# Kernel tuning notes

Measured on AMD Instinct MI355X. Metric: run time of the kernel, lower is better.

Reference implementation:

```python
import jax, jax.numpy as jnp
import numpy as np

NUM_HEADS = 32
NUM_KV_HEADS = 8
HEAD_DIM = 128
ROPE_THETA = 10000.0
NEG_INF = -1e9


def _rope_cos_sin(position_ids, head_dim, dtype):
    # inv_freq: [head_dim/2]
    inv_freq = 1.0 / (ROPE_THETA ** (jnp.arange(0, head_dim, 2, dtype=jnp.float32) / head_dim))
    # freqs: [B, S, head_dim/2]
    freqs = position_ids.astype(jnp.float32)[..., None] * inv_freq[None, None, :]
    emb = jnp.concatenate([freqs, freqs], axis=-1)  # [B, S, head_dim]
    return jnp.cos(emb).astype(dtype), jnp.sin(emb).astype(dtype)


def _rotate_half(x):
    x1, x2 = jnp.split(x, 2, axis=-1)
    return jnp.concatenate([-x2, x1], axis=-1)


def setup_inputs() -> dict:
    key = jax.random.key(0)
    k1, k2, k3, k4, k5 = jax.random.split(key, 5)
    B, S, H = 2, 2048, 4096
    scale = 1.0 / np.sqrt(H)
    return {
        "hidden_states": jax.random.normal(k1, (B, S, H), jnp.float32),
        "position_ids": jnp.broadcast_to(jnp.arange(S, dtype=jnp.int32)[None, :], (B, S)),
        "Wq": jax.random.normal(k2, (H, H), jnp.float32) * scale,
        "Wk": jax.random.normal(k3, (NUM_KV_HEADS * HEAD_DIM, H), jnp.float32) * scale,
        "Wv": jax.random.normal(k4, (NUM_KV_HEADS * HEAD_DIM, H), jnp.float32) * scale,
        "Wo": jax.random.normal(k5, (H, H), jnp.float32) * scale,
    }


def reference(hidden_states, position_ids, Wq, Wk, Wv, Wo):
    B, S, H = hidden_states.shape
    dtype = hidden_states.dtype
    n_rep = NUM_HEADS // NUM_KV_HEADS

    # QKV projections (torch Linear: x @ W.T)
    q = (hidden_states @ Wq.T).reshape(B, S, NUM_HEADS, HEAD_DIM).transpose(0, 2, 1, 3)
    k = (hidden_states @ Wk.T).reshape(B, S, NUM_KV_HEADS, HEAD_DIM).transpose(0, 2, 1, 3)
    v = (hidden_states @ Wv.T).reshape(B, S, NUM_KV_HEADS, HEAD_DIM).transpose(0, 2, 1, 3)

    # RoPE (cos/sin broadcast over heads)
    cos, sin = _rope_cos_sin(position_ids, HEAD_DIM, dtype)
    cos, sin = cos[:, None, :, :], sin[:, None, :, :]  # [B,1,S,D]
    q = q * cos + _rotate_half(q) * sin
    k = k * cos + _rotate_half(k) * sin

    # repeat_kv (GQA): [B, KVH, S, D] -> [B, KVH*n_rep, S, D]
    k = jnp.repeat(k, n_rep, axis=1)
    v = jnp.repeat(v, n_rep, axis=1)

    # scaled dot-product attention with causal mask, softmax in fp32
    scores = jnp.einsum('bhqd,bhkd->bhqk', q, k) / np.sqrt(HEAD_DIM)
    causal = jnp.tril(jnp.ones((S, S), dtype=bool))
    scores = jnp.where(causal[None, None, :, :], scores, NEG_INF)
    probs = jax.nn.softmax(scores.astype(jnp.float32), axis=-1).astype(dtype)

    attn = jnp.einsum('bhqk,bhkd->bhqd', probs, v)
    attn = attn.transpose(0, 2, 1, 3).reshape(B, S, H)
    return attn @ Wo.T
```

## Files before the change

kernel.cpp:

```cpp
#include <hip/hip_runtime.h>

#define S_LEN 2048
#define BATCH 2
#define HID 4096
#define NH 32
#define NKV 8
#define DH 128
#define MROWS (BATCH*S_LEN)
#define QKV_N 6144

typedef unsigned short u16;
typedef unsigned int u32;
typedef __bf16 bf16x8 __attribute__((ext_vector_type(8)));
typedef float f32x4 __attribute__((ext_vector_type(4)));
typedef u16 u16x8 __attribute__((ext_vector_type(8)));

__device__ __forceinline__ u16 f2bf(float f) {
  union { float f; u32 u; } v; v.f = f;
  return (u16)((v.u + 0x8000u) >> 16);
}
__device__ __forceinline__ float bf2f(u16 h) {
  union { u32 u; float f; } v; v.u = ((u32)h) << 16;
  return v.f;
}
__device__ __forceinline__ u32 cvtpk(float a, float b) {
  u32 r;
  asm("v_cvt_pk_bf16_f32 %0, %1, %2" : "=v"(r) : "v"(a), "v"(b));
  return r;
}
__device__ __forceinline__ void async16(const void* g, void* l) {
  __builtin_amdgcn_global_load_lds(
      (const __attribute__((address_space(1))) u32*)g,
      (__attribute__((address_space(3))) u32*)l, 16, 0, 0);
}
__device__ __forceinline__ f32x4 mfma16(bf16x8 a, bf16x8 b, f32x4 c) {
  return __builtin_amdgcn_mfma_f32_16x16x32_bf16(a, b, c, 0, 0, 0);
}

__global__ __launch_bounds__(256) void cvt_f32_bf16(const float* __restrict__ in,
                                                    u16* __restrict__ out, int n) {
  int i0 = (blockIdx.x * 256 + threadIdx.x) * 8;
  if (i0 >= n) return;
  float4 a = *(const float4*)(in + i0);
  float4 b = *(const float4*)(in + i0 + 4);
  u16x8 r;
  r[0]=f2bf(a.x); r[1]=f2bf(a.y); r[2]=f2bf(a.z); r[3]=f2bf(a.w);
  r[4]=f2bf(b.x); r[5]=f2bf(b.y); r[6]=f2bf(b.z); r[7]=f2bf(b.w);
  *(u16x8*)(out + i0) = r;
}

template<int OUT_BF16>
__global__ __launch_bounds__(512, 2) void gemm256(
    const u16* __restrict__ A, const u16* __restrict__ B, void* __restrict__ Cout,
    int M, int N, int K, int XC, int SR, int SC) {
  __shared__ u16 As[2][2][64 * 128];
  __shared__ u16 Bs[2][2][64 * 128];
  const int NKT = K >> 6;
  int bid = (int)blockIdx.x;
  int xcd = bid & 7, l = bid >> 3;
  int tm = (xcd / XC) * SR + l / SC;
  int tn = (xcd % XC) * SC + l % SC;
  int m0 = tm << 8, n0 = tn << 8;
  int t = threadIdx.x;
  int w = t >> 6, lane = t & 63, lo = lane & 15, hi = lane >> 4;
  int wm = w >> 2, wn = w & 3;
  int rbb = (wn & 1) << 6;

  int srow = (w << 3) + (lane >> 3);
  int scol = (lane & 7) << 3;

  auto stageA = [&](int kt, int buf, int h) {
#pragma unroll
    for (int c2 = 0; c2 < 2; ++c2) {
      int row = (c2 << 6) + srow;
      int col = scol ^ ((row & 7) << 3);
      async16(A + (size_t)(m0 + (h << 7) + row) * K + (kt << 6) + col,
              (char*)&As[buf][h][0] + (c2 << 13) + (w << 10));
    }
  };
  auto stageB = [&](int kt, int buf, int h) {
#pragma unroll
    for (int c2 = 0; c2 < 2; ++c2) {
      int row = (c2 << 6) + srow;
      int col = scol ^ ((row & 7) << 3);
      async16(B + (size_t)(n0 + (h << 7) + row) * K + (kt << 6) + col,
              (char*)&Bs[buf][h][0] + (c2 << 13) + (w << 10));
    }
  };

  const f32x4 fz = {0.f, 0.f, 0.f, 0.f};
  f32x4 acc[8][4];
#pragma unroll
  for (int i = 0; i < 8; ++i)
#pragma unroll
    for (int j = 0; j < 4; ++j) acc[i][j] = fz;
  bf16x8 af[4][2], bf0[2][2], bf1[2][2];

  auto rdA = [&](int c, int half, bf16x8 (&dst)[4][2]) {
    const u16* Ab = &As[c][wm][0];
#pragma unroll
    for (int mf = 0; mf < 4; ++mf)
#pragma unroll
      for (int ks = 0; ks < 2; ++ks) {
        int ra = (half << 6) + (mf << 4) + lo;
        dst[mf][ks] = *(const bf16x8*)(Ab + (ra << 6) +
                      (((ks << 5) + (hi << 3)) ^ ((ra & 7) << 3)));
      }
  };
  auto rdB = [&](int c, int bfrag, bf16x8 (&dst)[2][2]) {
    const u16* Bb = &Bs[c][wn >> 1][0];
#pragma unroll
    for (int nf = 0; nf < 2; ++nf)
#pragma unroll
      for (int ks = 0; ks < 2; ++ks) {
        int rb = rbb + (bfrag << 5) + (nf << 4) + lo;
        dst[nf][ks] = *(const bf16x8*)(Bb + (rb << 6) +
                      (((ks << 5) + (hi << 3)) ^ ((rb & 7) << 3)));
      }
  };
  auto MM = [&](bf16x8 (&a)[4][2], bf16x8 (&b)[2][2], int mo, int no) {
#pragma unroll
    for (int mf = 0; mf < 4; ++mf)
#pragma unroll
      for (int nf = 0; nf < 2; ++nf)
#pragma unroll
        for (int ks = 0; ks < 2; ++ks)
          acc[mo + mf][no + nf] = mfma16(a[mf][ks], b[nf][ks], acc[mo + mf][no + nf]);
  };

  stageA(0, 0, 0); stageA(0, 0, 1);
  stageB(0, 0, 0); stageB(0, 0, 1);
  stageB(1, 1, 0); stageB(1, 1, 1);
  asm volatile("s_waitcnt vmcnt(4)" ::: "memory");
  __builtin_amdgcn_s_barrier();
  rdA(0, 0, af);
  rdB(0, 0, bf0);

  for (int kt = 0; kt < NKT; ++kt) {
    int c = kt & 1;
    int kn1 = (kt + 1 == NKT) ? 0 : kt + 1;
    int kn2 = (kt + 2 >= NKT) ? kt + 2 - NKT : kt + 2;

    rdB(c, 1, bf1);
    stageA(kn1, c ^ 1, 0); stageA(kn1, c ^ 1, 1);
    __builtin_amdgcn_s_barrier();
    __builtin_amdgcn_s_setprio(1);
    MM(af, bf0, 0, 0);
    __builtin_amdgcn_s_setprio(0);
    __builtin_amdgcn_s_barrier();

    __builtin_amdgcn_s_setprio(1);
    MM(af, bf1, 0, 2);
    __builtin_amdgcn_s_setprio(0);
    rdA(c, 1, af);
    __builtin_amdgcn_s_barrier();

    stageB(kn2, c, 0);
    __builtin_amdgcn_s_barrier();
    __builtin_amdgcn_s_setprio(1);
    MM(af, bf1, 4, 2);
    __builtin_amdgcn_s_setprio(0);
    asm volatile("s_waitcnt vmcnt(2)" ::: "memory");
    __builtin_amdgcn_s_barrier();

    stageB(kn2, c, 1);
    __builtin_amdgcn_s_barrier();
    __builtin_amdgcn_s_setprio(1);
    MM(af, bf0, 4, 0);
    __builtin_amdgcn_s_setprio(0);
    rdA(c ^ 1, 0, af);
    rdB(c ^ 1, 0, bf0);
    __builtin_amdgcn_s_barrier();
  }

#pragma unroll
  for (int mf = 0; mf < 8; ++mf)
#pragma unroll
    for (int nf = 0; nf < 4; ++nf)
#pragma unroll
      for (int r = 0; r < 4; ++r) {
        int row = m0 + (wm << 7) + (mf << 4) + (hi << 2) + r;
        int col = n0 + (wn << 6) + (nf << 4) + lo;
        if (OUT_BF16) ((u16*)Cout)[(size_t)row * N + col] = f2bf(acc[mf][nf][r]);
        else          ((float*)Cout)[(size_t)row * N + col] = acc[mf][nf][r];
      }
}

__global__ __launch_bounds__(256) void rope_kernel(u16* __restrict__ X,
                                                   const int* __restrict__ pos,
                                                   int ncols, int pitch, float scale) {
  int idx = blockIdx.x * 256 + threadIdx.x;
  int groups = ncols >> 3;
  int m = idx / groups;
  int gi = idx - m * groups;
  if (m >= MROWS) return;
  int head = gi >> 4;
  int d0 = (gi & 15) << 2;
  float p = (float)pos[m];
  u16* base = X + (size_t)m * pitch + head * 128;
  u16 xa[4], xb[4], oa[4], ob[4];
  *(uint2*)xa = *(const uint2*)(base + d0);
  *(uint2*)xb = *(const uint2*)(base + d0 + 64);
#pragma unroll
  for (int i = 0; i < 4; ++i) {
    float j = (float)(d0 + i);
    float inv = __expf(j * -0.14391156516030342f);
    float fr = p * inv;
    float s, c;
    sincosf(fr, &s, &c);
    float x1 = bf2f(xa[i]), x2 = bf2f(xb[i]);
    oa[i] = f2bf((x1 * c - x2 * s) * scale);
    ob[i] = f2bf((x2 * c + x1 * s) * scale);
  }
  *(uint2*)(base + d0) = *(uint2*)oa;
  *(uint2*)(base + d0 + 64) = *(uint2*)ob;
}

__global__ __launch_bounds__(256) void transpose_v(const u16* __restrict__ V,
                                                   u16* __restrict__ Vt) {
  int bid = blockIdx.x;
  int s0 = (bid & 31) << 6;
  int bg = bid >> 5;
  int b = bg >> 3, g = bg & 7;
  __shared__ u16 tile[64][128];
  int t = threadIdx.x;
#pragma unroll
  for (int r = 0; r < 4; ++r) {
    int c = (r << 8) + t;
    int row = c >> 4, cc = c & 15;
    *(uint4*)&tile[row][cc * 8] =
        *(const uint4*)(V + (size_t)(b * S_LEN + s0 + row) * QKV_N + g * 128 + cc * 8);
  }
  __syncthreads();
#pragma unroll
  for (int r = 0; r < 4; ++r) {
    int c = (r << 8) + t;
    int d = c >> 3, cs = c & 7;
    u16 tmp[8];
#pragma unroll
    for (int i = 0; i < 8; ++i) tmp[i] = tile[cs * 8 + i][d];
    *(uint4*)(Vt + ((size_t)bg * 128 + d) * S_LEN + s0 + cs * 8) = *(uint4*)tmp;
  }
}

__global__ __launch_bounds__(256) void attn_kernel(
    const u16* __restrict__ Q, const u16* __restrict__ K,
    const u16* __restrict__ Vt, u16* __restrict__ O) {
  int bid = blockIdx.x;
  int qt = 31 - (bid >> 6);
  int bh = bid & 63;
  int b = bh >> 5, h = bh & 31;
  int g = h >> 2;
  __shared__ u16 Kl[64 * 128];
  __shared__ u16 Vl[128 * 64];
  __shared__ u16 Pl[4][16 * 72];
  int t = threadIdx.x, w = t >> 6, lane = t & 63, lo = lane & 15, hi = lane >> 4;

  bf16x8 qf[4];
  {
    const u16* qb = Q + (size_t)(b * S_LEN + (qt << 6) + (w << 4) + lo) * QKV_N + h * 128;
#pragma unroll
    for (int kk = 0; kk < 4; ++kk) qf[kk] = *(const bf16x8*)(qb + kk * 32 + hi * 8);
  }
  const f32x4 fz = {0.f, 0.f, 0.f, 0.f};
  f32x4 acc[8];
#pragma unroll
  for (int f = 0; f < 8; ++f) acc[f] = fz;
  float mrun = -1e30f, lrun = 0.f;

  const u16* Kbase = K + (size_t)(b * S_LEN) * QKV_N + g * 128;
  const u16* Vbase = Vt + (size_t)((b << 3) + g) * 128 * S_LEN;

  int ntiles = qt + 1;
  for (int tile = 0; tile < ntiles; ++tile) {
    int s0 = tile << 6;
#pragma unroll
    for (int r = 0; r < 4; ++r) {
      int c = (r << 8) + (w << 6) + lane;
      int row = c >> 4, cc = c & 15;
      int src = cc ^ (row & 7);
      async16(Kbase + (size_t)(s0 + row) * QKV_N + src * 8,
              (char*)Kl + (r << 12) + (w << 10));
    }
#pragma unroll
    for (int r = 0; r < 4; ++r) {
      int c = (r << 8) + (w << 6) + lane;
      int row = c >> 3, cc = c & 7;
      int src = cc ^ (row & 7);
      async16(Vbase + (size_t)row * S_LEN + s0 + src * 8,
              (char*)Vl + (r << 12) + (w << 10));
    }
    __syncthreads();

    f32x4 sf[4];
#pragma unroll
    for (int j = 0; j < 4; ++j) {
      f32x4 sv = fz;
#pragma unroll
      for (int kk = 0; kk < 4; ++kk) {
        int row = (j << 4) + lo;
        int ch = ((kk << 2) + hi) ^ (row & 7);
        bf16x8 kf = *(const bf16x8*)(Kl + row * 128 + ch * 8);
        sv = __builtin_amdgcn_mfma_f32_16x16x32_bf16(kf, qf[kk], sv, 0, 0, 0);
      }
      sf[j] = sv;
    }
    if (tile == qt) {
      int q_rel = (w << 4) + lo;
#pragma unroll
      for (int j = 0; j < 4; ++j)
#pragma unroll
        for (int r = 0; r < 4; ++r)
          if (((j << 4) + (hi << 2) + r) > q_rel) sf[j][r] = -1e9f;
    }
    float pmax = sf[0][0];
#pragma unroll
    for (int j = 0; j < 4; ++j)
#pragma unroll
      for (int r = 0; r < 4; ++r) pmax = fmaxf(pmax, sf[j][r]);
    pmax = fmaxf(pmax, __shfl_xor(pmax, 16, 64));
    pmax = fmaxf(pmax, __shfl_xor(pmax, 32, 64));
    if (__any(pmax > mrun + 8.f)) {
      float mn = fmaxf(mrun, pmax);
      float fsc = __expf(mrun - mn);
      mrun = mn;
      lrun *= fsc;
#pragma unroll
      for (int f = 0; f < 8; ++f)
#pragma unroll
        for (int r = 0; r < 4; ++r) acc[f][r] *= fsc;
    }
    float psum = 0.f;
#pragma unroll
    for (int j = 0; j < 4; ++j)
#pragma unroll
      for (int r = 0; r < 4; ++r) {
        float p = __expf(sf[j][r] - mrun);
        sf[j][r] = p;
        psum += p;
      }
    psum += __shfl_xor(psum, 16, 64);
    psum += __shfl_xor(psum, 32, 64);
    lrun += psum;

#pragma unroll
    for (int j = 0; j < 4; ++j) {
      uint2 pk;
      pk.x = cvtpk(sf[j][0], sf[j][1]);
      pk.y = cvtpk(sf[j][2], sf[j][3]);
      *(uint2*)&Pl[w][lo * 72 + (j << 4) + (hi << 2)] = pk;
    }
#pragma unroll
    for (int kk = 0; kk < 2; ++kk) {
      bf16x8 pf = *(const bf16x8*)&Pl[w][lo * 72 + (kk << 5) + (hi << 3)];
#pragma unroll
      for (int f = 0; f < 8; ++f) {
        int vrow = (f << 4) + lo;
        int phys = ((kk << 2) + hi) ^ (vrow & 7);
        bf16x8 vf = *(const bf16x8*)(Vl + vrow * 64 + phys * 8);
        acc[f] = __builtin_amdgcn_mfma_f32_16x16x32_bf16(vf, pf, acc[f], 0, 0, 0);
      }
    }
    __syncthreads();
  }

  float rl = 1.0f / lrun;
#pragma unroll
  for (int half = 0; half < 2; ++half) {
#pragma unroll
    for (int f2 = 0; f2 < 4; ++f2) {
      int f = (half << 2) + f2;
      uint2 pk;
      pk.x = cvtpk(acc[f][0] * rl, acc[f][1] * rl);
      pk.y = cvtpk(acc[f][2] * rl, acc[f][3] * rl);
      *(uint2*)&Pl[w][lo * 72 + (f2 << 4) + (hi << 2)] = pk;
    }
#pragma unroll
    for (int it = 0; it < 2; ++it) {
      int rowq = (lane >> 3) + (it << 3);
      int c8 = lane & 7;
      uint4 val = *(const uint4*)&Pl[w][rowq * 72 + c8 * 8];
      *(uint4*)(O + (size_t)(b * S_LEN + (qt << 6) + (w << 4) + rowq) * 4096 +
                h * 128 + (half << 6) + c8 * 8) = val;
    }
  }
}

extern "C" void kernel_launch(void* const* d_in, const int* in_sizes, int n_in,
                              void* d_out, int out_size, void* d_ws, size_t ws_size,
                              hipStream_t stream) {
  const float* hidden = (const float*)d_in[0];
  const int* pos = (const int*)d_in[1];
  const float* Wq = (const float*)d_in[2];
  const float* Wk = (const float*)d_in[3];
  const float* Wv = (const float*)d_in[4];
  const float* Wo = (const float*)d_in[5];
  float* out = (float*)d_out;

  u16* hb   = (u16*)d_ws;
  u16* wqb  = hb   + 16777216;
  u16* wkb  = wqb  + 16777216;
  u16* wvb  = wkb  + 4194304;
  u16* wob  = wvb  + 4194304;
  u16* QKVb = wob  + 16777216;
  u16* Vtb  = QKVb + 25165824;
  u16* Ob   = Vtb  + 4194304;

  cvt_f32_bf16<<<8192, 256, 0, stream>>>(hidden, hb, 16777216);
  cvt_f32_bf16<<<8192, 256, 0, stream>>>(Wq, wqb, 16777216);
  cvt_f32_bf16<<<2048, 256, 0, stream>>>(Wk, wkb, 4194304);
  cvt_f32_bf16<<<2048, 256, 0, stream>>>(Wv, wvb, 4194304);
  cvt_f32_bf16<<<8192, 256, 0, stream>>>(Wo, wob, 16777216);

  gemm256<1><<<384, 512, 0, stream>>>(hb, wqb, QKVb, 4096, QKV_N, 4096, 4, 8, 6);

  rope_kernel<<<8192, 256, 0, stream>>>(QKVb, pos, 4096, QKV_N, 0.08838834764831845f);
  rope_kernel<<<2048, 256, 0, stream>>>(QKVb + 4096, pos, 1024, QKV_N, 1.0f);

  transpose_v<<<512, 256, 0, stream>>>(QKVb + 5120, Vtb);

  attn_kernel<<<2048, 256, 0, stream>>>(QKVb, QKVb + 4096, Vtb, Ob);

  gemm256<0><<<256, 512, 0, stream>>>(Ob, wob, out, 4096, 4096, 4096, 2, 4, 8);
}
```

Baseline: 536.0 us.

## Replace 256x256 GEMM tiles with 128x128 tiles using 4 warps

```diff
diff --git a/kernel.cpp b/kernel.cpp
--- a/kernel.cpp
+++ b/kernel.cpp
@@ -50,136 +50,119 @@
 }
 
 template<int OUT_BF16>
-__global__ __launch_bounds__(512, 2) void gemm256(
+__global__ __launch_bounds__(256, 2) void gemm128(
     const u16* __restrict__ A, const u16* __restrict__ B, void* __restrict__ Cout,
     int M, int N, int K, int XC, int SR, int SC) {
-  __shared__ u16 As[2][2][64 * 128];
-  __shared__ u16 Bs[2][2][64 * 128];
+  __shared__ u16 As[2][128 * 64];
+  __shared__ u16 Bs[2][128 * 64];
   const int NKT = K >> 6;
   int bid = (int)blockIdx.x;
   int xcd = bid & 7, l = bid >> 3;
   int tm = (xcd / XC) * SR + l / SC;
   int tn = (xcd % XC) * SC + l % SC;
-  int m0 = tm << 8, n0 = tn << 8;
+  int m0 = tm << 7, n0 = tn << 7;
   int t = threadIdx.x;
   int w = t >> 6, lane = t & 63, lo = lane & 15, hi = lane >> 4;
-  int wm = w >> 2, wn = w & 3;
-  int rbb = (wn & 1) << 6;
-
-  int srow = (w << 3) + (lane >> 3);
-  int scol = (lane & 7) << 3;
-
-  auto stageA = [&](int kt, int buf, int h) {
-#pragma unroll
-    for (int c2 = 0; c2 < 2; ++c2) {
-      int row = (c2 << 6) + srow;
-      int col = scol ^ ((row & 7) << 3);
-      async16(A + (size_t)(m0 + (h << 7) + row) * K + (kt << 6) + col,
-              (char*)&As[buf][h][0] + (c2 << 13) + (w << 10));
+  int wm = w >> 1, wn = w & 1;
+
+  int srow_t = t >> 3;
+  int schunk = t & 7;
+
+  auto stageA = [&](int kt, int buf) {
+#pragma unroll
+    for (int r = 0; r < 4; ++r) {
+      int row = (r << 5) + srow_t;
+      int src = schunk ^ (row & 7);
+      async16(A + (size_t)(m0 + row) * K + (kt << 6) + src * 8,
+              (char*)&As[buf][0] + (r << 12) + (w << 10));
     }
   };
-  auto stageB = [&](int kt, int buf, int h) {
-#pragma unroll
-    for (int c2 = 0; c2 < 2; ++c2) {
-      int row = (c2 << 6) + srow;
-      int col = scol ^ ((row & 7) << 3);
-      async16(B + (size_t)(n0 + (h << 7) + row) * K + (kt << 6) + col,
-              (char*)&Bs[buf][h][0] + (c2 << 13) + (w << 10));
+  auto stageB = [&](int kt, int buf) {
+#pragma unroll
+    for (int r = 0; r < 4; ++r) {
+      int row = (r << 5) + srow_t;
+      int src = schunk ^ (row & 7);
+      async16(B + (size_t)(n0 + row) * K + (kt << 6) + src * 8,
+              (char*)&Bs[buf][0] + (r << 12) + (w << 10));
     }
   };
 
   const f32x4 fz = {0.f, 0.f, 0.f, 0.f};
-  f32x4 acc[8][4];
-#pragma unroll
-  for (int i = 0; i < 8; ++i)
+  f32x4 acc[4][4];
+#pragma unroll
+  for (int i = 0; i < 4; ++i)
 #pragma unroll
     for (int j = 0; j < 4; ++j) acc[i][j] = fz;
-  bf16x8 af[4][2], bf0[2][2], bf1[2][2];
-
-  auto rdA = [&](int c, int half, bf16x8 (&dst)[4][2]) {
-    const u16* Ab = &As[c][wm][0];
+  bf16x8 af[4][2], bfL[2][2], bfR[2][2];
+
+  auto rdA = [&](int c, bf16x8 (&dst)[4][2]) {
+    const u16* Ab = &As[c][0];
 #pragma unroll
     for (int mf = 0; mf < 4; ++mf)
 #pragma unroll
       for (int ks = 0; ks < 2; ++ks) {
-        int ra = (half << 6) + (mf << 4) + lo;
-        dst[mf][ks] = *(const bf16x8*)(Ab + (ra << 6) +
-                      (((ks << 5) + (hi << 3)) ^ ((ra & 7) << 3)));
+        int ra = (wm << 6) + (mf << 4) + lo;
+        dst[mf][ks] = *(const bf16x8*)(Ab + ra * 64 +
+                      ((((ks << 2) + hi) ^ (ra & 7)) << 3));
       }
   };
-  auto rdB = [&](int c, int bfrag, bf16x8 (&dst)[2][2]) {
-    const u16* Bb = &Bs[c][wn >> 1][0];
+  auto rdBh = [&](int c, int half, bf16x8 (&dst)[2][2]) {
+    const u16* Bb = &Bs[c][0];
 #pragma unroll
     for (int nf = 0; nf < 2; ++nf)
 #pragma unroll
       for (int ks = 0; ks < 2; ++ks) {
-        int rb = rbb + (bfrag << 5) + (nf << 4) + lo;
-        dst[nf][ks] = *(const bf16x8*)(Bb + (rb << 6) +
-                      (((ks << 5) + (hi << 3)) ^ ((rb & 7) << 3)));
+        int rb = (wn << 6) + (half << 5) + (nf << 4) + lo;
+        dst[nf][ks] = *(const bf16x8*)(Bb + rb * 64 +
+                      ((((ks << 2) + hi) ^ (rb & 7)) << 3));
       }
   };
-  auto MM = [&](bf16x8 (&a)[4][2], bf16x8 (&b)[2][2], int mo, int no) {
+  auto MM = [&](bf16x8 (&a)[4][2], bf16x8 (&b)[2][2], int no) {
 #pragma unroll
     for (int mf = 0; mf < 4; ++mf)
 #pragma unroll
       for (int nf = 0; nf < 2; ++nf)
 #pragma unroll
         for (int ks = 0; ks < 2; ++ks)
-          acc[mo + mf][no + nf] = mfma16(a[mf][ks], b[nf][ks], acc[mo + mf][no + nf]);
+          acc[mf][no + nf] = mfma16(a[mf][ks], b[nf][ks], acc[mf][no + nf]);
   };
 
-  stageA(0, 0, 0); stageA(0, 0, 1);
-  stageB(0, 0, 0); stageB(0, 0, 1);
-  stageB(1, 1, 0); stageB(1, 1, 1);
-  asm volatile("s_waitcnt vmcnt(4)" ::: "memory");
+  stageA(0, 0); stageB(0, 0);
+  stageA(1, 1); stageB(1, 1);
+  asm volatile("s_waitcnt vmcnt(8)" ::: "memory");
   __builtin_amdgcn_s_barrier();
-  rdA(0, 0, af);
-  rdB(0, 0, bf0);
+  rdA(0, af);
+  rdBh(0, 0, bfL);
 
   for (int kt = 0; kt < NKT; ++kt) {
     int c = kt & 1;
-    int kn1 = (kt + 1 == NKT) ? 0 : kt + 1;
-    int kn2 = (kt + 2 >= NKT) ? kt + 2 - NKT : kt + 2;
-
-    rdB(c, 1, bf1);
-    stageA(kn1, c ^ 1, 0); stageA(kn1, c ^ 1, 1);
+    int kn2 = kt + 2; if (kn2 >= NKT) kn2 -= NKT;
+
+    rdBh(c, 1, bfR);
     __builtin_amdgcn_s_barrier();
     __builtin_amdgcn_s_setprio(1);
-    MM(af, bf0, 0, 0);
+    MM(af, bfL, 0);
     __builtin_amdgcn_s_setprio(0);
     __builtin_amdgcn_s_barrier();
 
-    __builtin_amdgcn_s_setprio(1);
-    MM(af, bf1, 0, 2);
-    __builtin_amdgcn_s_setprio(0);
-    rdA(c, 1, af);
-    __builtin_amdgcn_s_barrier();
-
-    stageB(kn2, c, 0);
+    stageA(kn2, c); stageB(kn2, c);
     __builtin_amdgcn_s_barrier();
     __builtin_amdgcn_s_setprio(1);
-    MM(af, bf1, 4, 2);
+    MM(af, bfR, 2);
     __builtin_amdgcn_s_setprio(0);
-    asm volatile("s_waitcnt vmcnt(2)" ::: "memory");
+    asm volatile("s_waitcnt vmcnt(8)" ::: "memory");
     __builtin_amdgcn_s_barrier();
-
-    stageB(kn2, c, 1);
-    __builtin_amdgcn_s_barrier();
-    __builtin_amdgcn_s_setprio(1);
-    MM(af, bf0, 4, 0);
-    __builtin_amdgcn_s_setprio(0);
-    rdA(c ^ 1, 0, af);
-    rdB(c ^ 1, 0, bf0);
-    __builtin_amdgcn_s_barrier();
-  }
-
-#pragma unroll
-  for (int mf = 0; mf < 8; ++mf)
+    rdA(c ^ 1, af);
+    rdBh(c ^ 1, 0, bfL);
+  }
+
+#pragma unroll
+  for (int mf = 0; mf < 4; ++mf)
 #pragma unroll
     for (int nf = 0; nf < 4; ++nf)
 #pragma unroll
       for (int r = 0; r < 4; ++r) {
-        int row = m0 + (wm << 7) + (mf << 4) + (hi << 2) + r;
+        int row = m0 + (wm << 6) + (mf << 4) + (hi << 2) + r;
         int col = n0 + (wn << 6) + (nf << 4) + lo;
         if (OUT_BF16) ((u16*)Cout)[(size_t)row * N + col] = f2bf(acc[mf][nf][r]);
         else          ((float*)Cout)[(size_t)row * N + col] = acc[mf][nf][r];
@@ -412,7 +395,7 @@
   cvt_f32_bf16<<<2048, 256, 0, stream>>>(Wv, wvb, 4194304);
   cvt_f32_bf16<<<8192, 256, 0, stream>>>(Wo, wob, 16777216);
 
-  gemm256<1><<<384, 512, 0, stream>>>(hb, wqb, QKVb, 4096, QKV_N, 4096, 4, 8, 6);
+  gemm128<1><<<1536, 256, 0, stream>>>(hb, wqb, QKVb, 4096, QKV_N, 4096, 4, 16, 12);
 
   rope_kernel<<<8192, 256, 0, stream>>>(QKVb, pos, 4096, QKV_N, 0.08838834764831845f);
   rope_kernel<<<2048, 256, 0, stream>>>(QKVb + 4096, pos, 1024, QKV_N, 1.0f);
@@ -421,5 +404,5 @@
 
   attn_kernel<<<2048, 256, 0, stream>>>(QKVb, QKVb + 4096, Vtb, Ob);
 
-  gemm256<0><<<256, 512, 0, stream>>>(Ob, wob, out, 4096, 4096, 4096, 2, 4, 8);
-}
+  gemm128<0><<<1024, 256, 0, stream>>>(Ob, wob, out, 4096, 4096, 4096, 2, 8, 16);
+}
```

Result: slower. 565.0 us (+5.4%).

## Restructure GEMM main loop into unrolled two-stage pipeline with explicit LDS waits

Applied to the files above, without the earlier changes.

```diff
diff --git a/kernel.cpp b/kernel.cpp
--- a/kernel.cpp
+++ b/kernel.cpp
@@ -128,50 +128,74 @@
           acc[mo + mf][no + nf] = mfma16(a[mf][ks], b[nf][ks], acc[mo + mf][no + nf]);
   };
 
+#define BAR()    __builtin_amdgcn_s_barrier()
+#define LGKM0()  asm volatile("s_waitcnt lgkmcnt(0)" ::: "memory")
+#define VM4()    asm volatile("s_waitcnt vmcnt(4)" ::: "memory")
+#define PRIO(x)  __builtin_amdgcn_s_setprio(x)
+
   stageA(0, 0, 0); stageA(0, 0, 1);
   stageB(0, 0, 0); stageB(0, 0, 1);
   stageB(1, 1, 0); stageB(1, 1, 1);
-  asm volatile("s_waitcnt vmcnt(4)" ::: "memory");
-  __builtin_amdgcn_s_barrier();
-  rdA(0, 0, af);
-  rdB(0, 0, bf0);
-
-  for (int kt = 0; kt < NKT; ++kt) {
-    int c = kt & 1;
-    int kn1 = (kt + 1 == NKT) ? 0 : kt + 1;
-    int kn2 = (kt + 2 >= NKT) ? kt + 2 - NKT : kt + 2;
-
-    rdB(c, 1, bf1);
-    stageA(kn1, c ^ 1, 0); stageA(kn1, c ^ 1, 1);
-    __builtin_amdgcn_s_barrier();
-    __builtin_amdgcn_s_setprio(1);
+  VM4();
+  BAR();
+
+  const int NT = NKT >> 1;
+  for (int it = 0; it < NT; ++it) {
+    int e = it << 1, o = e + 1;
+    int e2 = (e + 2 >= NKT) ? 0 : e + 2;
+    int o2 = (o + 2 >= NKT) ? 1 : o + 2;
+
+    rdA(0, 0, af); rdB(0, 0, bf0);
+    stageA(o, 1, 0);
+    BAR(); LGKM0(); PRIO(1);
     MM(af, bf0, 0, 0);
-    __builtin_amdgcn_s_setprio(0);
-    __builtin_amdgcn_s_barrier();
-
-    __builtin_amdgcn_s_setprio(1);
+    PRIO(0); BAR();
+
+    rdB(0, 1, bf1);
+    stageA(o, 1, 1);
+    BAR(); LGKM0(); PRIO(1);
     MM(af, bf1, 0, 2);
-    __builtin_amdgcn_s_setprio(0);
-    rdA(c, 1, af);
-    __builtin_amdgcn_s_barrier();
-
-    stageB(kn2, c, 0);
-    __builtin_amdgcn_s_barrier();
-    __builtin_amdgcn_s_setprio(1);
+    PRIO(0); BAR();
+
+    rdA(0, 1, af);
+    stageB(e2, 0, 0);
+    BAR(); LGKM0(); PRIO(1);
     MM(af, bf1, 4, 2);
-    __builtin_amdgcn_s_setprio(0);
-    asm volatile("s_waitcnt vmcnt(2)" ::: "memory");
-    __builtin_amdgcn_s_barrier();
-
-    stageB(kn2, c, 1);
-    __builtin_amdgcn_s_barrier();
-    __builtin_amdgcn_s_setprio(1);
+    PRIO(0); BAR();
+
+    stageB(e2, 0, 1);
+    BAR(); PRIO(1);
     MM(af, bf0, 4, 0);
-    __builtin_amdgcn_s_setprio(0);
-    rdA(c ^ 1, 0, af);
-    rdB(c ^ 1, 0, bf0);
-    __builtin_amdgcn_s_barrier();
-  }
+    PRIO(0); VM4(); BAR();
+
+    rdA(1, 0, af); rdB(1, 0, bf0);
+    stageA(e2, 0, 0);
+    BAR(); LGKM0(); PRIO(1);
+    MM(af, bf0, 0, 0);
+    PRIO(0); BAR();
+
+    rdB(1, 1, bf1);
+    stageA(e2, 0, 1);
+    BAR(); LGKM0(); PRIO(1);
+    MM(af, bf1, 0, 2);
+    PRIO(0); BAR();
+
+    rdA(1, 1, af);
+    stageB(o2, 1, 0);
+    BAR(); LGKM0(); PRIO(1);
+    MM(af, bf1, 4, 2);
+    PRIO(0); BAR();
+
+    stageB(o2, 1, 1);
+    BAR(); PRIO(1);
+    MM(af, bf0, 4, 0);
+    PRIO(0); VM4(); BAR();
+  }
+
+#undef BAR
+#undef LGKM0
+#undef VM4
+#undef PRIO
 
 #pragma unroll
   for (int mf = 0; mf < 8; ++mf)
```

Measured after the change: 539.3 us. No clear change (+0.6%).
